# Kernel optimization log

Hardware: AMD Instinct MI355X
Metric: run time of the kernel (lower is better)

Reference implementation:

```python
import jax, jax.numpy as jnp
import numpy as np

IN_C, HID, LSTM_H, OUT_C = 128, 128, 128, 2
N_NODES, N_EDGES, N_GRAPHS = 100000, 1600000, 256


def gcn_conv(x, src, dst, W, b, n_nodes):
    # h = XW, then symmetric-normalized aggregation with self loops (PyG GCNConv defaults)
    h = x @ W  # [N, H]
    loop = jnp.arange(n_nodes)
    s = jnp.concatenate([src, loop])
    d = jnp.concatenate([dst, loop])
    deg = jax.ops.segment_sum(jnp.ones_like(d, dtype=h.dtype), d, num_segments=n_nodes)
    dinv = jnp.where(deg > 0, jax.lax.rsqrt(deg), 0.0)
    norm = dinv[s] * dinv[d]  # [E+N]
    out = jax.ops.segment_sum(norm[:, None] * h[s], d, num_segments=n_nodes)
    return out + b


def setup_inputs() -> dict:
    key = jax.random.key(0)
    ks = jax.random.split(key, 16)
    x = jax.random.normal(ks[0], (N_NODES, IN_C), dtype=jnp.float32)
    edge_index = jax.random.randint(ks[1], (2, N_EDGES), 0, N_NODES)
    batch = jnp.sort(jax.random.randint(ks[2], (N_NODES,), 0, N_GRAPHS))
    sc = lambda *shape: 1.0 / np.sqrt(shape[0])
    W0 = jax.random.normal(ks[3], (IN_C, HID), jnp.float32) * sc(IN_C)
    b0 = jnp.zeros((HID,), jnp.float32)
    W1 = jax.random.normal(ks[4], (HID, HID), jnp.float32) * sc(HID)
    b1 = jnp.zeros((HID,), jnp.float32)
    W2 = jax.random.normal(ks[5], (HID, HID), jnp.float32) * sc(HID)
    b2 = jnp.zeros((HID,), jnp.float32)
    W_ih = jax.random.normal(ks[6], (4 * LSTM_H, HID), jnp.float32) * sc(HID)
    W_hh = jax.random.normal(ks[7], (4 * LSTM_H, LSTM_H), jnp.float32) * sc(LSTM_H)
    b_ih = jnp.zeros((4 * LSTM_H,), jnp.float32)
    b_hh = jnp.zeros((4 * LSTM_H,), jnp.float32)
    W_fc = jax.random.normal(ks[8], (OUT_C, LSTM_H), jnp.float32) * sc(LSTM_H)
    b_fc = jnp.zeros((OUT_C,), jnp.float32)
    return dict(x=x, edge_index=edge_index, batch=batch, num_graphs=N_GRAPHS,
                W0=W0, b0=b0, W1=W1, b1=b1, W2=W2, b2=b2,
                W_ih=W_ih, W_hh=W_hh, b_ih=b_ih, b_hh=b_hh, W_fc=W_fc, b_fc=b_fc)


def reference(x, edge_index, batch, num_graphs, W0, b0, W1, b1, W2, b2,
              W_ih, W_hh, b_ih, b_hh, W_fc, b_fc):
    n_nodes = x.shape[0]
    src, dst = edge_index[0], edge_index[1]
    h = x
    for W, b in ((W0, b0), (W1, b1), (W2, b2)):
        h = jax.nn.relu(gcn_conv(h, src, dst, W, b, n_nodes))
    # dropout: identity in eval mode
    # global_mean_pool over batch ids
    sums = jax.ops.segment_sum(h, batch, num_segments=num_graphs)  # [G, HID]
    cnts = jax.ops.segment_sum(jnp.ones((n_nodes,), h.dtype), batch, num_segments=num_graphs)
    pooled = sums / jnp.maximum(cnts, 1.0)[:, None]
    # single-step LSTM from zero state: h0 = c0 = 0 => W_hh contributes 0
    g = pooled @ W_ih.T + b_ih + b_hh  # [G, 4H]
    i, f, gg, o = jnp.split(g, 4, axis=-1)  # PyTorch gate order i,f,g,o
    c = jax.nn.sigmoid(i) * jnp.tanh(gg)
    hn = jax.nn.sigmoid(o) * jnp.tanh(c)
    return hn @ W_fc.T + b_fc
```

## Files before the change

kernel.cpp:

```cpp
#include <hip/hip_runtime.h>
#include <math.h>
#include <stdint.h>

#define HID 128
#define SCAN_CHUNK 1024
#define NBUCK_MAX 512
#define EDGE_TILE 8192
#define GEMM_ROWS 128
#define XS_STRIDE 136

typedef short bf16x8 __attribute__((ext_vector_type(8)));
typedef float f32x4 __attribute__((ext_vector_type(4)));

__device__ __forceinline__ unsigned int f2bf(float f) {
    union { float f; uint32_t i; } u; u.f = f;
    uint32_t r = u.i + 0x7fffu + ((u.i >> 16) & 1u);
    return r >> 16;
}

__global__ __launch_bounds__(256) void scan_phase1(const int* __restrict__ cnt,
                                                   int* __restrict__ blockSums,
                                                   float* __restrict__ dinv, int nN) {
    __shared__ int sdata[256];
    const int t = threadIdx.x;
    const int idx = blockIdx.x * SCAN_CHUNK + t * 4;
    int v0 = 0, v1 = 0, v2 = 0, v3 = 0;
    if (idx + 3 < nN) {
        int4 v = *(const int4*)(cnt + idx);
        v0 = v.x; v1 = v.y; v2 = v.z; v3 = v.w;
        float4 dv;
        dv.x = rsqrtf((float)v0 + 1.0f);
        dv.y = rsqrtf((float)v1 + 1.0f);
        dv.z = rsqrtf((float)v2 + 1.0f);
        dv.w = rsqrtf((float)v3 + 1.0f);
        *(float4*)(dinv + idx) = dv;
    } else {
        if (idx     < nN) { v0 = cnt[idx];     dinv[idx]     = rsqrtf((float)v0 + 1.0f); }
        if (idx + 1 < nN) { v1 = cnt[idx + 1]; dinv[idx + 1] = rsqrtf((float)v1 + 1.0f); }
        if (idx + 2 < nN) { v2 = cnt[idx + 2]; dinv[idx + 2] = rsqrtf((float)v2 + 1.0f); }
        if (idx + 3 < nN) { v3 = cnt[idx + 3]; dinv[idx + 3] = rsqrtf((float)v3 + 1.0f); }
    }
    sdata[t] = v0 + v1 + v2 + v3;
    __syncthreads();
#pragma unroll
    for (int off = 128; off > 0; off >>= 1) {
        if (t < off) sdata[t] += sdata[t + off];
        __syncthreads();
    }
    if (t == 0) blockSums[blockIdx.x] = sdata[0];
}

__global__ __launch_bounds__(256) void scan_phase2(int* __restrict__ blockSums, int nB) {
    __shared__ int sd[256];
    const int t = threadIdx.x;
    sd[t] = (t < nB) ? blockSums[t] : 0;
    __syncthreads();
#pragma unroll
    for (int off = 1; off < 256; off <<= 1) {
        int v = sd[t];
        int add = (t >= off) ? sd[t - off] : 0;
        __syncthreads();
        sd[t] = v + add;
        __syncthreads();
    }
    if (t < nB) blockSums[t] = (t > 0) ? sd[t - 1] : 0;
}

__global__ __launch_bounds__(256) void scan_phase3(const int* __restrict__ cnt,
                                                   const int* __restrict__ blockOffsets,
                                                   int* __restrict__ rowptr, int nN, int nE) {
    __shared__ int sdata[256];
    const int t = threadIdx.x;
    const int idx = blockIdx.x * SCAN_CHUNK + t * 4;
    int v0 = 0, v1 = 0, v2 = 0, v3 = 0;
    if (idx + 3 < nN) {
        int4 v = *(const int4*)(cnt + idx);
        v0 = v.x; v1 = v.y; v2 = v.z; v3 = v.w;
    } else {
        if (idx     < nN) v0 = cnt[idx];
        if (idx + 1 < nN) v1 = cnt[idx + 1];
        if (idx + 2 < nN) v2 = cnt[idx + 2];
        if (idx + 3 < nN) v3 = cnt[idx + 3];
    }
    sdata[t] = v0 + v1 + v2 + v3;
    __syncthreads();
#pragma unroll
    for (int off = 1; off < 256; off <<= 1) {
        int v = sdata[t];
        int add = (t >= off) ? sdata[t - off] : 0;
        __syncthreads();
        sdata[t] = v + add;
        __syncthreads();
    }
    const int pre = blockOffsets[blockIdx.x] + ((t > 0) ? sdata[t - 1] : 0);
    if (idx + 3 < nN) {
        *(int4*)(rowptr + idx) = make_int4(pre, pre + v0, pre + v0 + v1, pre + v0 + v1 + v2);
    } else {
        if (idx     < nN) rowptr[idx]     = pre;
        if (idx + 1 < nN) rowptr[idx + 1] = pre + v0;
        if (idx + 2 < nN) rowptr[idx + 2] = pre + v0 + v1;
        if (idx + 3 < nN) rowptr[idx + 3] = pre + v0 + v1 + v2;
    }
    if (blockIdx.x == 0 && t == 0) rowptr[nN] = nE;
}

__global__ __launch_bounds__(256) void bucket_count(const int* __restrict__ dst,
                                                    int* __restrict__ bcnt, int nE, int nB) {
    __shared__ int h[NBUCK_MAX];
    for (int i = threadIdx.x; i < nB; i += 256) h[i] = 0;
    __syncthreads();
    const int base = blockIdx.x * EDGE_TILE;
    const int end = min(base + EDGE_TILE, nE);
    for (int e = base + threadIdx.x; e < end; e += 256)
        atomicAdd(&h[dst[e] >> 8], 1);
    __syncthreads();
    for (int i = threadIdx.x; i < nB; i += 256)
        if (h[i]) atomicAdd(&bcnt[i], h[i]);
}

__global__ __launch_bounds__(512) void bucket_scan(const int* __restrict__ bcnt,
                                                   int* __restrict__ boff,
                                                   int* __restrict__ bcur, int nB) {
    __shared__ int sd[512];
    const int t = threadIdx.x;
    sd[t] = (t < nB) ? bcnt[t] : 0;
    __syncthreads();
#pragma unroll
    for (int off = 1; off < 512; off <<= 1) {
        int v = sd[t];
        int add = (t >= off) ? sd[t - off] : 0;
        __syncthreads();
        sd[t] = v + add;
        __syncthreads();
    }
    if (t < nB) {
        int ex = (t > 0) ? sd[t - 1] : 0;
        boff[t] = ex;
        bcur[t] = ex;
    }
}

__global__ __launch_bounds__(256) void bucket_scatter(const int* __restrict__ src,
                                                      const int* __restrict__ dst,
                                                      int* __restrict__ bcur,
                                                      uint2* __restrict__ ebuf, int nE, int nB) {
    __shared__ int h[NBUCK_MAX];
    __shared__ int basearr[NBUCK_MAX];
    const int base = blockIdx.x * EDGE_TILE;
    const int end = min(base + EDGE_TILE, nE);
    for (int i = threadIdx.x; i < nB; i += 256) h[i] = 0;
    __syncthreads();
    for (int e = base + threadIdx.x; e < end; e += 256)
        atomicAdd(&h[dst[e] >> 8], 1);
    __syncthreads();
    for (int i = threadIdx.x; i < nB; i += 256) {
        int c = h[i];
        basearr[i] = c ? atomicAdd(&bcur[i], c) : 0;
        h[i] = 0;
    }
    __syncthreads();
    for (int e = base + threadIdx.x; e < end; e += 256) {
        int d = dst[e];
        int b = d >> 8;
        int pos = basearr[b] + atomicAdd(&h[b], 1);
        ebuf[pos] = make_uint2((unsigned)src[e], (unsigned)d);
    }
}

__global__ __launch_bounds__(256) void node_count(const uint2* __restrict__ ebuf,
                                                  const int* __restrict__ boff,
                                                  int* __restrict__ cnt, int nE, int nB, int nN) {
    __shared__ int h[256];
    h[threadIdx.x] = 0;
    __syncthreads();
    const int b = blockIdx.x;
    const int e0 = boff[b];
    const int e1 = (b + 1 < nB) ? boff[b + 1] : nE;
    for (int e = e0 + threadIdx.x; e < e1; e += 256)
        atomicAdd(&h[ebuf[e].y & 255], 1);
    __syncthreads();
    const int v = b * 256 + threadIdx.x;
    if (v < nN) cnt[v] = h[threadIdx.x];
}

__global__ __launch_bounds__(256) void csr_from_buckets(const uint2* __restrict__ ebuf,
                                                        const int* __restrict__ boff,
                                                        const int* __restrict__ rowptr,
                                                        int* __restrict__ ssrc, int nE, int nB) {
    __shared__ int cur[256];
    const int b = blockIdx.x;
    const int e0 = boff[b];
    const int e1 = (b + 1 < nB) ? boff[b + 1] : nE;
    cur[threadIdx.x] = 0;
    __syncthreads();
    for (int e = e0 + threadIdx.x; e < e1; e += 256) {
        uint2 ed = ebuf[e];
        int d = (int)ed.y;
        int pos = rowptr[d] + atomicAdd(&cur[d & 255], 1);
        ssrc[pos] = (int)ed.x;
    }
}

__global__ __launch_bounds__(256) void xcvt_kernel(const float* __restrict__ x,
                                                   uint4* __restrict__ Xb, int total) {
    int i = blockIdx.x * 256 + threadIdx.x;
    if (i < total) {
        const float4* xp = (const float4*)x + (size_t)i * 2;
        float4 u = xp[0], v = xp[1];
        uint4 o;
        o.x = f2bf(u.x) | (f2bf(u.y) << 16);
        o.y = f2bf(u.z) | (f2bf(u.w) << 16);
        o.z = f2bf(v.x) | (f2bf(v.y) << 16);
        o.w = f2bf(v.z) | (f2bf(v.w) << 16);
        Xb[i] = o;
    }
}

__global__ __launch_bounds__(256) void wt_kernel(const float* __restrict__ W0,
                                                 const float* __restrict__ W1,
                                                 const float* __restrict__ W2,
                                                 unsigned short* __restrict__ Wtb) {
    int i = blockIdx.x * 256 + threadIdx.x;
    if (i < 3 * HID * HID) {
        int w = i >> 14, r = i & 16383;
        int n = r >> 7, k = r & 127;
        const float* W = (w == 0) ? W0 : (w == 1) ? W1 : W2;
        Wtb[i] = (unsigned short)f2bf(W[k * HID + n]);
    }
}

__global__ __launch_bounds__(256) void gemm_mfma_kernel(const uint4* __restrict__ Xb,
                                                        const uint4* __restrict__ Wtb,
                                                        const float* __restrict__ dinv,
                                                        unsigned int* __restrict__ Pb32,
                                                        int nN) {
    __shared__ short Xs[GEMM_ROWS * XS_STRIDE];
    __shared__ short Ws[HID * XS_STRIDE];
    const int tid = threadIdx.x;
    const int rowBase = blockIdx.x * GEMM_ROWS;
#pragma unroll
    for (int it = 0; it < 8; ++it) {
        int f = it * 256 + tid;
        int row = f >> 4, c = f & 15;
        uint4 v = Xb[(size_t)(rowBase + row) * 16 + c];
        *(uint4*)(&Xs[row * XS_STRIDE + c * 8]) = v;
    }
#pragma unroll
    for (int it = 0; it < 8; ++it) {
        int f = it * 256 + tid;
        int n = f >> 4, c = f & 15;
        *(uint4*)(&Ws[n * XS_STRIDE + c * 8]) = Wtb[f];
    }
    __syncthreads();
    const int wave = tid >> 6, lane = tid & 63;
    const int quad = lane >> 4, l16 = lane & 15;
    f32x4 acc[2][8] = {};
    const int kq = quad * 8;
#pragma unroll
    for (int ks = 0; ks < 4; ++ks) {
        const int k0 = ks * 32 + kq;
        bf16x8 a0 = *(const bf16x8*)(&Xs[(wave * 32 + l16) * XS_STRIDE + k0]);
        bf16x8 a1 = *(const bf16x8*)(&Xs[(wave * 32 + 16 + l16) * XS_STRIDE + k0]);
#pragma unroll
        for (int nt = 0; nt < 8; ++nt) {
            bf16x8 b = *(const bf16x8*)(&Ws[(nt * 16 + l16) * XS_STRIDE + k0]);
            acc[0][nt] = __builtin_amdgcn_mfma_f32_16x16x32_bf16(a0, b, acc[0][nt], 0, 0, 0);
            acc[1][nt] = __builtin_amdgcn_mfma_f32_16x16x32_bf16(a1, b, acc[1][nt], 0, 0, 0);
        }
    }
#pragma unroll
    for (int mt = 0; mt < 2; ++mt) {
        const int gr0 = rowBase + wave * 32 + mt * 16 + quad * 4;
#pragma unroll
        for (int r = 0; r < 4; ++r) {
            const int gr = gr0 + r;
            const bool ok = gr < nN;
            const float d = ok ? dinv[gr] : 0.f;
#pragma unroll
            for (int nt = 0; nt < 8; ++nt) {
                float v = d * acc[mt][nt][r];
                float vo = __shfl_xor(v, 1, 64);
                if (ok && !(l16 & 1)) {
                    Pb32[(size_t)gr * 64 + nt * 8 + (l16 >> 1)] = f2bf(v) | (f2bf(vo) << 16);
                }
            }
        }
    }
}

__device__ __forceinline__ void acc_bf8(const uint4 q, float* a) {
    union { uint32_t i; float f; } t;
    t.i = q.x << 16;          a[0] += t.f;
    t.i = q.x & 0xffff0000u;  a[1] += t.f;
    t.i = q.y << 16;          a[2] += t.f;
    t.i = q.y & 0xffff0000u;  a[3] += t.f;
    t.i = q.z << 16;          a[4] += t.f;
    t.i = q.z & 0xffff0000u;  a[5] += t.f;
    t.i = q.w << 16;          a[6] += t.f;
    t.i = q.w & 0xffff0000u;  a[7] += t.f;
}

__global__ __launch_bounds__(256) void agg_kernel(const uint4* __restrict__ Pb,
                                                  const int* __restrict__ rowptr,
                                                  const int* __restrict__ ssrc,
                                                  const float* __restrict__ dinv,
                                                  const float* __restrict__ bias,
                                                  uint4* __restrict__ Xb_out, int nN) {
    const int lane = threadIdx.x & 15;
    const int grp = threadIdx.x >> 4;
    const int v = blockIdx.x * 16 + grp;
    if (v >= nN) return;
    float a0[8], a1[8], a2[8], a3[8];
#pragma unroll
    for (int i = 0; i < 8; ++i) { a0[i] = 0.f; a1[i] = 0.f; a2[i] = 0.f; a3[i] = 0.f; }
    acc_bf8(Pb[(size_t)v * 16 + lane], a0);
    int e = rowptr[v];
    const int e1 = rowptr[v + 1];
    for (; e + 4 <= e1; e += 4) {
        const int u0 = ssrc[e + 0], u1 = ssrc[e + 1], u2 = ssrc[e + 2], u3 = ssrc[e + 3];
        uint4 q0 = Pb[(size_t)u0 * 16 + lane];
        uint4 q1 = Pb[(size_t)u1 * 16 + lane];
        uint4 q2 = Pb[(size_t)u2 * 16 + lane];
        uint4 q3 = Pb[(size_t)u3 * 16 + lane];
        acc_bf8(q0, a0); acc_bf8(q1, a1); acc_bf8(q2, a2); acc_bf8(q3, a3);
    }
    for (; e < e1; ++e) {
        uint4 q = Pb[(size_t)ssrc[e] * 16 + lane];
        acc_bf8(q, a1);
    }
    const float dv = dinv[v];
    const float4 bb0 = ((const float4*)bias)[lane * 2];
    const float4 bb1 = ((const float4*)bias)[lane * 2 + 1];
    float4 o0, o1;
    o0.x = fmaxf(fmaf(dv, (a0[0] + a1[0]) + (a2[0] + a3[0]), bb0.x), 0.f);
    o0.y = fmaxf(fmaf(dv, (a0[1] + a1[1]) + (a2[1] + a3[1]), bb0.y), 0.f);
    o0.z = fmaxf(fmaf(dv, (a0[2] + a1[2]) + (a2[2] + a3[2]), bb0.z), 0.f);
    o0.w = fmaxf(fmaf(dv, (a0[3] + a1[3]) + (a2[3] + a3[3]), bb0.w), 0.f);
    o1.x = fmaxf(fmaf(dv, (a0[4] + a1[4]) + (a2[4] + a3[4]), bb1.x), 0.f);
    o1.y = fmaxf(fmaf(dv, (a0[5] + a1[5]) + (a2[5] + a3[5]), bb1.y), 0.f);
    o1.z = fmaxf(fmaf(dv, (a0[6] + a1[6]) + (a2[6] + a3[6]), bb1.z), 0.f);
    o1.w = fmaxf(fmaf(dv, (a0[7] + a1[7]) + (a2[7] + a3[7]), bb1.w), 0.f);
    uint4 q;
    q.x = f2bf(o0.x) | (f2bf(o0.y) << 16);
    q.y = f2bf(o0.z) | (f2bf(o0.w) << 16);
    q.z = f2bf(o1.x) | (f2bf(o1.y) << 16);
    q.w = f2bf(o1.z) | (f2bf(o1.w) << 16);
    Xb_out[(size_t)v * 16 + lane] = q;
}

__global__ __launch_bounds__(256) void pool_partial(const unsigned int* __restrict__ Xb32,
                                                    const int* __restrict__ batch,
                                                    float* __restrict__ psum, int nN) {
    const int c2 = threadIdx.x & 63;
    int n = blockIdx.x * 64 + (threadIdx.x >> 6);
    const int nEnd = min(blockIdx.x * 64 + 64, nN);
    float acc0 = 0.f, acc1 = 0.f;
    int g = -1;
    for (; n < nEnd; n += 4) {
        int gn = batch[n];
        unsigned int q = Xb32[(size_t)n * 64 + c2];
        union { uint32_t i; float f; } lo, hi;
        lo.i = q << 16; hi.i = q & 0xffff0000u;
        if (gn != g) {
            if (g >= 0) {
                atomicAdd(&psum[g * HID + c2 * 2], acc0);
                atomicAdd(&psum[g * HID + c2 * 2 + 1], acc1);
            }
            g = gn;
            acc0 = lo.f; acc1 = hi.f;
        } else {
            acc0 += lo.f; acc1 += hi.f;
        }
    }
    if (g >= 0) {
        atomicAdd(&psum[g * HID + c2 * 2], acc0);
        atomicAdd(&psum[g * HID + c2 * 2 + 1], acc1);
    }
}

__global__ __launch_bounds__(128) void pool_finalize(const float* __restrict__ psum,
                                                     const int* __restrict__ batch,
                                                     float* __restrict__ pooled, int nN) {
    const int g = blockIdx.x;
    int lo = 0, hi = nN;
    while (lo < hi) { int m = (lo + hi) >> 1; if (batch[m] < g) lo = m + 1; else hi = m; }
    const int start = lo;
    hi = nN;
    while (lo < hi) { int m = (lo + hi) >> 1; if (batch[m] < g + 1) lo = m + 1; else hi = m; }
    const float c = (float)max(lo - start, 1);
    pooled[g * HID + threadIdx.x] = psum[g * HID + threadIdx.x] / c;
}

__device__ __forceinline__ float sigmoidf_(float x) { return 1.0f / (1.0f + expf(-x)); }

__global__ __launch_bounds__(128) void lstm_fc_kernel(const float* __restrict__ pooled,
                                                      const float* __restrict__ W_ih,
                                                      const float* __restrict__ b_ih,
                                                      const float* __restrict__ b_hh,
                                                      const float* __restrict__ W_fc,
                                                      const float* __restrict__ b_fc,
                                                      float* __restrict__ out) {
    __shared__ float pv[HID];
    __shared__ float r0[2], r1[2];
    const int g = blockIdx.x, j = threadIdx.x;
    pv[j] = pooled[g * HID + j];
    __syncthreads();
    float di = b_ih[j] + b_hh[j];
    float dg = b_ih[256 + j] + b_hh[256 + j];
    float dO = b_ih[384 + j] + b_hh[384 + j];
    const float4* pv4 = (const float4*)pv;
#pragma unroll 4
    for (int k4 = 0; k4 < 32; ++k4) {
        float4 p = pv4[k4];
        float4 wi = *(const float4*)(W_ih + (size_t)j * HID + k4 * 4);
        float4 wg = *(const float4*)(W_ih + (size_t)(256 + j) * HID + k4 * 4);
        float4 wo = *(const float4*)(W_ih + (size_t)(384 + j) * HID + k4 * 4);
        di += p.x * wi.x + p.y * wi.y + p.z * wi.z + p.w * wi.w;
        dg += p.x * wg.x + p.y * wg.y + p.z * wg.z + p.w * wg.w;
        dO += p.x * wo.x + p.y * wo.y + p.z * wo.z + p.w * wo.w;
    }
    float c = sigmoidf_(di) * tanhf(dg);
    float hn = sigmoidf_(dO) * tanhf(c);
    float p0 = hn * W_fc[j];
    float p1 = hn * W_fc[HID + j];
#pragma unroll
    for (int off = 32; off > 0; off >>= 1) {
        p0 += __shfl_down(p0, off, 64);
        p1 += __shfl_down(p1, off, 64);
    }
    const int w = j >> 6, l = j & 63;
    if (l == 0) { r0[w] = p0; r1[w] = p1; }
    __syncthreads();
    if (j == 0) {
        out[g * 2 + 0] = r0[0] + r0[1] + b_fc[0];
        out[g * 2 + 1] = r1[0] + r1[1] + b_fc[1];
    }
}

extern "C" void kernel_launch(void* const* d_in, const int* in_sizes, int n_in,
                              void* d_out, int out_size, void* d_ws, size_t ws_size,
                              hipStream_t stream) {
    const float* x      = (const float*)d_in[0];
    const int*   eidx   = (const int*)d_in[1];
    const int*   batch  = (const int*)d_in[2];
    const float* W0     = (const float*)d_in[4];
    const float* b0     = (const float*)d_in[5];
    const float* W1     = (const float*)d_in[6];
    const float* b1     = (const float*)d_in[7];
    const float* W2     = (const float*)d_in[8];
    const float* b2     = (const float*)d_in[9];
    const float* W_ih   = (const float*)d_in[10];
    const float* b_ih   = (const float*)d_in[12];
    const float* b_hh   = (const float*)d_in[13];
    const float* W_fc   = (const float*)d_in[14];
    const float* b_fc   = (const float*)d_in[15];
    float* out = (float*)d_out;

    const int nN = in_sizes[0] / HID;
    const int nE = in_sizes[1] / 2;
    const int nG = out_size / 2;
    const int* src = eidx;
    const int* dst = eidx + nE;
    const int rowsPad = (nN + GEMM_ROWS - 1) & ~(GEMM_ROWS - 1);

    size_t off = 0;
    auto alloc = [&](size_t bytes) -> void* {
        void* p = (char*)d_ws + off;
        off += (bytes + 255) & ~(size_t)255;
        return p;
    };
    uint4* Pb     = (uint4*)alloc((size_t)rowsPad * 16 * sizeof(uint4));
    uint4* Xb     = (uint4*)alloc((size_t)nN * 16 * sizeof(uint4));
    float* dinv   = (float*)alloc((size_t)nN * sizeof(float));
    int*   cnt    = (int*)alloc((size_t)nN * sizeof(int));
    int*   rowptr = (int*)alloc((size_t)(nN + 1) * sizeof(int));
    int*   ssrc   = (int*)alloc((size_t)nE * sizeof(int));
    uint2* ebuf   = (uint2*)alloc((size_t)nE * sizeof(uint2));
    float* pooled = (float*)alloc((size_t)nG * HID * sizeof(float));
    float* psum   = (float*)alloc((size_t)nG * HID * sizeof(float));
    int*   blockSums = (int*)alloc(1024 * sizeof(int));
    int*   bcnt   = (int*)alloc(NBUCK_MAX * sizeof(int));
    int*   boff   = (int*)alloc(NBUCK_MAX * sizeof(int));
    int*   bcur   = (int*)alloc(NBUCK_MAX * sizeof(int));
    unsigned short* Wtb = (unsigned short*)alloc(3 * HID * HID * sizeof(unsigned short));
    (void)ws_size;

    const int scanBlocks = (nN + SCAN_CHUNK - 1) / SCAN_CHUNK;
    const int nB = (nN + 255) >> 8;
    const int tileBlocks = (nE + EDGE_TILE - 1) / EDGE_TILE;

    hipMemsetAsync(bcnt, 0, NBUCK_MAX * sizeof(int), stream);
    bucket_count<<<tileBlocks, 256, 0, stream>>>(dst, bcnt, nE, nB);
    bucket_scan<<<1, 512, 0, stream>>>(bcnt, boff, bcur, nB);
    bucket_scatter<<<tileBlocks, 256, 0, stream>>>(src, dst, bcur, ebuf, nE, nB);

    node_count<<<nB, 256, 0, stream>>>(ebuf, boff, cnt, nE, nB, nN);
    scan_phase1<<<scanBlocks, 256, 0, stream>>>(cnt, blockSums, dinv, nN);
    scan_phase2<<<1, 256, 0, stream>>>(blockSums, scanBlocks);
    scan_phase3<<<scanBlocks, 256, 0, stream>>>(cnt, blockSums, rowptr, nN, nE);
    csr_from_buckets<<<nB, 256, 0, stream>>>(ebuf, boff, rowptr, ssrc, nE, nB);

    const int xTotal = nN * 16;
    xcvt_kernel<<<(xTotal + 255) / 256, 256, 0, stream>>>(x, Xb, xTotal);
    wt_kernel<<<(3 * HID * HID + 255) / 256, 256, 0, stream>>>(W0, W1, W2, Wtb);

    const int gemmBlocks = rowsPad / GEMM_ROWS;
    const int aggBlocks = (nN + 15) / 16;
    const uint4* Wt0 = (const uint4*)Wtb;
    const uint4* Wt1 = (const uint4*)(Wtb + HID * HID);
    const uint4* Wt2 = (const uint4*)(Wtb + 2 * HID * HID);

    gemm_mfma_kernel<<<gemmBlocks, 256, 0, stream>>>(Xb, Wt0, dinv, (unsigned int*)Pb, nN);
    agg_kernel<<<aggBlocks, 256, 0, stream>>>(Pb, rowptr, ssrc, dinv, b0, Xb, nN);
    gemm_mfma_kernel<<<gemmBlocks, 256, 0, stream>>>(Xb, Wt1, dinv, (unsigned int*)Pb, nN);
    agg_kernel<<<aggBlocks, 256, 0, stream>>>(Pb, rowptr, ssrc, dinv, b1, Xb, nN);
    gemm_mfma_kernel<<<gemmBlocks, 256, 0, stream>>>(Xb, Wt2, dinv, (unsigned int*)Pb, nN);
    agg_kernel<<<aggBlocks, 256, 0, stream>>>(Pb, rowptr, ssrc, dinv, b2, Xb, nN);

    hipMemsetAsync(psum, 0, (size_t)nG * HID * sizeof(float), stream);
    pool_partial<<<(nN + 63) / 64, 256, 0, stream>>>((const unsigned int*)Xb, batch, psum, nN);
    pool_finalize<<<nG, 128, 0, stream>>>(psum, batch, pooled, nN);
    lstm_fc_kernel<<<nG, 128, 0, stream>>>(pooled, W_ih, b_ih, b_hh, W_fc, b_fc, out);
}
```

Measured before the change: 480.3 us.

## Split CSR neighbors by source half and fuse fp32-to-bf16 conversion into first GEMM

The CSR build now sorts each node's neighbor list into two segments, sources in the lower half of node ids and sources in the upper half, and records a per-node midpoint. The aggregation kernel walks the lower-half segment first and then the upper half, so gathers across all concurrently running waves concentrate on one half of the feature table at a time, aiming for better L2/MALL locality. The separate x-to-bf16 conversion kernel is removed, and a new first-layer GEMM reads the fp32 input and converts it while loading into shared memory; the GEMM also gains bounds checks on rows. The cost is an extra counting pass over edges in the CSR build, an extra rowmid array, and an outer loop in aggregation that may leave more remainder iterations.

```diff
diff --git a/kernel.cpp b/kernel.cpp
--- a/kernel.cpp
+++ b/kernel.cpp
@@ -186,33 +186,38 @@
 __global__ __launch_bounds__(256) void csr_from_buckets(const uint2* __restrict__ ebuf,
                                                         const int* __restrict__ boff,
                                                         const int* __restrict__ rowptr,
-                                                        int* __restrict__ ssrc, int nE, int nB) {
-    __shared__ int cur[256];
+                                                        int* __restrict__ rowmid,
+                                                        int* __restrict__ ssrc,
+                                                        int nE, int nB, int nN, int nHalf) {
+    __shared__ int rbase[256];
+    __shared__ int rmid[256];
+    __shared__ int cLow[256], cHigh[256];
+    const int t = threadIdx.x;
     const int b = blockIdx.x;
     const int e0 = boff[b];
     const int e1 = (b + 1 < nB) ? boff[b + 1] : nE;
-    cur[threadIdx.x] = 0;
-    __syncthreads();
-    for (int e = e0 + threadIdx.x; e < e1; e += 256) {
+    const int v = b * 256 + t;
+    rbase[t] = (v <= nN) ? rowptr[v] : 0;
+    cLow[t] = 0;
+    __syncthreads();
+    for (int e = e0 + t; e < e1; e += 256) {
         uint2 ed = ebuf[e];
-        int d = (int)ed.y;
-        int pos = rowptr[d] + atomicAdd(&cur[d & 255], 1);
-        ssrc[pos] = (int)ed.x;
-    }
-}
-
-__global__ __launch_bounds__(256) void xcvt_kernel(const float* __restrict__ x,
-                                                   uint4* __restrict__ Xb, int total) {
-    int i = blockIdx.x * 256 + threadIdx.x;
-    if (i < total) {
-        const float4* xp = (const float4*)x + (size_t)i * 2;
-        float4 u = xp[0], v = xp[1];
-        uint4 o;
-        o.x = f2bf(u.x) | (f2bf(u.y) << 16);
-        o.y = f2bf(u.z) | (f2bf(u.w) << 16);
-        o.z = f2bf(v.x) | (f2bf(v.y) << 16);
-        o.w = f2bf(v.z) | (f2bf(v.w) << 16);
-        Xb[i] = o;
+        if ((int)ed.x < nHalf) atomicAdd(&cLow[ed.y & 255], 1);
+    }
+    __syncthreads();
+    rmid[t] = rbase[t] + cLow[t];
+    if (v < nN) rowmid[v] = rmid[t];
+    cLow[t] = 0;
+    cHigh[t] = 0;
+    __syncthreads();
+    for (int e = e0 + t; e < e1; e += 256) {
+        uint2 ed = ebuf[e];
+        int li = (int)ed.y & 255;
+        int u = (int)ed.x;
+        int pos;
+        if (u < nHalf) pos = rbase[li] + atomicAdd(&cLow[li], 1);
+        else           pos = rmid[li] + atomicAdd(&cHigh[li], 1);
+        ssrc[pos] = u;
     }
 }
 
@@ -242,8 +247,74 @@
     for (int it = 0; it < 8; ++it) {
         int f = it * 256 + tid;
         int row = f >> 4, c = f & 15;
-        uint4 v = Xb[(size_t)(rowBase + row) * 16 + c];
+        int grow = rowBase + row;
+        uint4 v = make_uint4(0u, 0u, 0u, 0u);
+        if (grow < nN) v = Xb[(size_t)grow * 16 + c];
         *(uint4*)(&Xs[row * XS_STRIDE + c * 8]) = v;
+    }
+#pragma unroll
+    for (int it = 0; it < 8; ++it) {
+        int f = it * 256 + tid;
+        int n = f >> 4, c = f & 15;
+        *(uint4*)(&Ws[n * XS_STRIDE + c * 8]) = Wtb[f];
+    }
+    __syncthreads();
+    const int wave = tid >> 6, lane = tid & 63;
+    const int quad = lane >> 4, l16 = lane & 15;
+    f32x4 acc[2][8] = {};
+    const int kq = quad * 8;
+#pragma unroll
+    for (int ks = 0; ks < 4; ++ks) {
+        const int k0 = ks * 32 + kq;
+        bf16x8 a0 = *(const bf16x8*)(&Xs[(wave * 32 + l16) * XS_STRIDE + k0]);
+        bf16x8 a1 = *(const bf16x8*)(&Xs[(wave * 32 + 16 + l16) * XS_STRIDE + k0]);
+#pragma unroll
+        for (int nt = 0; nt < 8; ++nt) {
+            bf16x8 b = *(const bf16x8*)(&Ws[(nt * 16 + l16) * XS_STRIDE + k0]);
+            acc[0][nt] = __builtin_amdgcn_mfma_f32_16x16x32_bf16(a0, b, acc[0][nt], 0, 0, 0);
+            acc[1][nt] = __builtin_amdgcn_mfma_f32_16x16x32_bf16(a1, b, acc[1][nt], 0, 0, 0);
+        }
+    }
+#pragma unroll
+    for (int mt = 0; mt < 2; ++mt) {
+        const int gr0 = rowBase + wave * 32 + mt * 16 + quad * 4;
+#pragma unroll
+        for (int r = 0; r < 4; ++r) {
+            const int gr = gr0 + r;
+            const bool ok = gr < nN;
+            const float d = ok ? dinv[gr] : 0.f;
+#pragma unroll
+            for (int nt = 0; nt < 8; ++nt) {
+                float v = d * acc[mt][nt][r];
+                float vo = __shfl_xor(v, 1, 64);
+                if (ok && !(l16 & 1)) {
+                    Pb32[(size_t)gr * 64 + nt * 8 + (l16 >> 1)] = f2bf(v) | (f2bf(vo) << 16);
+                }
+            }
+        }
+    }
+}
+
+__global__ __launch_bounds__(256) void gemm_mfma_f32in(const float* __restrict__ X,
+                                                       const uint4* __restrict__ Wtb,
+                                                       const float* __restrict__ dinv,
+                                                       unsigned int* __restrict__ Pb32,
+                                                       int nN) {
+    __shared__ short Xs[GEMM_ROWS * XS_STRIDE];
+    __shared__ short Ws[HID * XS_STRIDE];
+    const int tid = threadIdx.x;
+    const int rowBase = blockIdx.x * GEMM_ROWS;
+#pragma unroll
+    for (int it = 0; it < 16; ++it) {
+        int f = it * 256 + tid;
+        int row = f >> 5, c = f & 31;
+        int grow = rowBase + row;
+        float4 v = make_float4(0.f, 0.f, 0.f, 0.f);
+        if (grow < nN) v = *(const float4*)(X + (size_t)grow * HID + c * 4);
+        uint2 o;
+        o.x = f2bf(v.x) | (f2bf(v.y) << 16);
+        o.y = f2bf(v.z) | (f2bf(v.w) << 16);
+        *(uint2*)(&Xs[row * XS_STRIDE + c * 4]) = o;
     }
 #pragma unroll
     for (int it = 0; it < 8; ++it) {
@@ -302,6 +373,7 @@
 
 __global__ __launch_bounds__(256) void agg_kernel(const uint4* __restrict__ Pb,
                                                   const int* __restrict__ rowptr,
+                                                  const int* __restrict__ rowmid,
                                                   const int* __restrict__ ssrc,
                                                   const float* __restrict__ dinv,
                                                   const float* __restrict__ bias,
@@ -314,19 +386,23 @@
 #pragma unroll
     for (int i = 0; i < 8; ++i) { a0[i] = 0.f; a1[i] = 0.f; a2[i] = 0.f; a3[i] = 0.f; }
     acc_bf8(Pb[(size_t)v * 16 + lane], a0);
-    int e = rowptr[v];
-    const int e1 = rowptr[v + 1];
-    for (; e + 4 <= e1; e += 4) {
-        const int u0 = ssrc[e + 0], u1 = ssrc[e + 1], u2 = ssrc[e + 2], u3 = ssrc[e + 3];
-        uint4 q0 = Pb[(size_t)u0 * 16 + lane];
-        uint4 q1 = Pb[(size_t)u1 * 16 + lane];
-        uint4 q2 = Pb[(size_t)u2 * 16 + lane];
-        uint4 q3 = Pb[(size_t)u3 * 16 + lane];
-        acc_bf8(q0, a0); acc_bf8(q1, a1); acc_bf8(q2, a2); acc_bf8(q3, a3);
-    }
-    for (; e < e1; ++e) {
-        uint4 q = Pb[(size_t)ssrc[e] * 16 + lane];
-        acc_bf8(q, a1);
+    const int ee0 = rowptr[v], em = rowmid[v], ee1 = rowptr[v + 1];
+#pragma unroll 1
+    for (int ph = 0; ph < 2; ++ph) {
+        int e = ph ? em : ee0;
+        const int eE = ph ? ee1 : em;
+        for (; e + 4 <= eE; e += 4) {
+            const int u0 = ssrc[e + 0], u1 = ssrc[e + 1], u2 = ssrc[e + 2], u3 = ssrc[e + 3];
+            uint4 q0 = Pb[(size_t)u0 * 16 + lane];
+            uint4 q1 = Pb[(size_t)u1 * 16 + lane];
+            uint4 q2 = Pb[(size_t)u2 * 16 + lane];
+            uint4 q3 = Pb[(size_t)u3 * 16 + lane];
+            acc_bf8(q0, a0); acc_bf8(q1, a1); acc_bf8(q2, a2); acc_bf8(q3, a3);
+        }
+        for (; e < eE; ++e) {
+            uint4 q = Pb[(size_t)ssrc[e] * 16 + lane];
+            acc_bf8(q, a1);
+        }
     }
     const float dv = dinv[v];
     const float4 bb0 = ((const float4*)bias)[lane * 2];
@@ -462,6 +538,7 @@
     const int* src = eidx;
     const int* dst = eidx + nE;
     const int rowsPad = (nN + GEMM_ROWS - 1) & ~(GEMM_ROWS - 1);
+    const int nHalf = nN >> 1;
 
     size_t off = 0;
     auto alloc = [&](size_t bytes) -> void* {
@@ -474,6 +551,7 @@
     float* dinv   = (float*)alloc((size_t)nN * sizeof(float));
     int*   cnt    = (int*)alloc((size_t)nN * sizeof(int));
     int*   rowptr = (int*)alloc((size_t)(nN + 1) * sizeof(int));
+    int*   rowmid = (int*)alloc((size_t)nN * sizeof(int));
     int*   ssrc   = (int*)alloc((size_t)nE * sizeof(int));
     uint2* ebuf   = (uint2*)alloc((size_t)nE * sizeof(uint2));
     float* pooled = (float*)alloc((size_t)nG * HID * sizeof(float));
@@ -498,10 +576,8 @@
     scan_phase1<<<scanBlocks, 256, 0, stream>>>(cnt, blockSums, dinv, nN);
     scan_phase2<<<1, 256, 0, stream>>>(blockSums, scanBlocks);
     scan_phase3<<<scanBlocks, 256, 0, stream>>>(cnt, blockSums, rowptr, nN, nE);
-    csr_from_buckets<<<nB, 256, 0, stream>>>(ebuf, boff, rowptr, ssrc, nE, nB);
-
-    const int xTotal = nN * 16;
-    xcvt_kernel<<<(xTotal + 255) / 256, 256, 0, stream>>>(x, Xb, xTotal);
+    csr_from_buckets<<<nB, 256, 0, stream>>>(ebuf, boff, rowptr, rowmid, ssrc, nE, nB, nN, nHalf);
+
     wt_kernel<<<(3 * HID * HID + 255) / 256, 256, 0, stream>>>(W0, W1, W2, Wtb);
 
     const int gemmBlocks = rowsPad / GEMM_ROWS;
@@ -510,12 +586,12 @@
     const uint4* Wt1 = (const uint4*)(Wtb + HID * HID);
     const uint4* Wt2 = (const uint4*)(Wtb + 2 * HID * HID);
 
-    gemm_mfma_kernel<<<gemmBlocks, 256, 0, stream>>>(Xb, Wt0, dinv, (unsigned int*)Pb, nN);
-    agg_kernel<<<aggBlocks, 256, 0, stream>>>(Pb, rowptr, ssrc, dinv, b0, Xb, nN);
+    gemm_mfma_f32in<<<gemmBlocks, 256, 0, stream>>>(x, Wt0, dinv, (unsigned int*)Pb, nN);
+    agg_kernel<<<aggBlocks, 256, 0, stream>>>(Pb, rowptr, rowmid, ssrc, dinv, b0, Xb, nN);
     gemm_mfma_kernel<<<gemmBlocks, 256, 0, stream>>>(Xb, Wt1, dinv, (unsigned int*)Pb, nN);
-    agg_kernel<<<aggBlocks, 256, 0, stream>>>(Pb, rowptr, ssrc, dinv, b1, Xb, nN);
+    agg_kernel<<<aggBlocks, 256, 0, stream>>>(Pb, rowptr, rowmid, ssrc, dinv, b1, Xb, nN);
     gemm_mfma_kernel<<<gemmBlocks, 256, 0, stream>>>(Xb, Wt2, dinv, (unsigned int*)Pb, nN);
-    agg_kernel<<<aggBlocks, 256, 0, stream>>>(Pb, rowptr, ssrc, dinv, b2, Xb, nN);
+    agg_kernel<<<aggBlocks, 256, 0, stream>>>(Pb, rowptr, rowmid, ssrc, dinv, b2, Xb, nN);
 
     hipMemsetAsync(psum, 0, (size_t)nG * HID * sizeof(float), stream);
     pool_partial<<<(nN + 63) / 64, 256, 0, stream>>>((const unsigned int*)Xb, batch, psum, nN);
```

Measured after the change: 478.6 us. No clear change (-0.4%).

## Fuse aggregation with next-layer GEMM, fold x conversion into GEMM, pack edge buffer

Applied to the files above, without the earlier changes.

The first GEMM now reads fp32 x and converts it to bf16 while staging, so the separate x conversion pass is gone. Layers 1 and 2 fuse the neighbour aggregation, bias and ReLU with the next layer's MFMA GEMM through a 16-row shared tile, which avoids writing and re-reading the intermediate activations. Ping-pong buffers Pb and Pb2 hold the projected features. Edge bucketing packs src<<8 | local dst into one 32-bit word, halving ebuf traffic, but this assumes source ids fit in 24 bits. Each fused block reloads the full 128x128 weight tile and runs only a small MFMA, adding per-block overhead.

```diff
diff --git a/kernel.cpp b/kernel.cpp
--- a/kernel.cpp
+++ b/kernel.cpp
@@ -143,7 +143,8 @@
 __global__ __launch_bounds__(256) void bucket_scatter(const int* __restrict__ src,
                                                       const int* __restrict__ dst,
                                                       int* __restrict__ bcur,
-                                                      uint2* __restrict__ ebuf, int nE, int nB) {
+                                                      unsigned int* __restrict__ ebuf,
+                                                      int nE, int nB) {
     __shared__ int h[NBUCK_MAX];
     __shared__ int basearr[NBUCK_MAX];
     const int base = blockIdx.x * EDGE_TILE;
@@ -163,11 +164,11 @@
         int d = dst[e];
         int b = d >> 8;
         int pos = basearr[b] + atomicAdd(&h[b], 1);
-        ebuf[pos] = make_uint2((unsigned)src[e], (unsigned)d);
-    }
-}
-
-__global__ __launch_bounds__(256) void node_count(const uint2* __restrict__ ebuf,
+        ebuf[pos] = ((unsigned)src[e] << 8) | ((unsigned)d & 255u);
+    }
+}
+
+__global__ __launch_bounds__(256) void node_count(const unsigned int* __restrict__ ebuf,
                                                   const int* __restrict__ boff,
                                                   int* __restrict__ cnt, int nE, int nB, int nN) {
     __shared__ int h[256];
@@ -177,13 +178,13 @@
     const int e0 = boff[b];
     const int e1 = (b + 1 < nB) ? boff[b + 1] : nE;
     for (int e = e0 + threadIdx.x; e < e1; e += 256)
-        atomicAdd(&h[ebuf[e].y & 255], 1);
+        atomicAdd(&h[ebuf[e] & 255u], 1);
     __syncthreads();
     const int v = b * 256 + threadIdx.x;
     if (v < nN) cnt[v] = h[threadIdx.x];
 }
 
-__global__ __launch_bounds__(256) void csr_from_buckets(const uint2* __restrict__ ebuf,
+__global__ __launch_bounds__(256) void csr_from_buckets(const unsigned int* __restrict__ ebuf,
                                                         const int* __restrict__ boff,
                                                         const int* __restrict__ rowptr,
                                                         int* __restrict__ ssrc, int nE, int nB) {
@@ -191,28 +192,14 @@
     const int b = blockIdx.x;
     const int e0 = boff[b];
     const int e1 = (b + 1 < nB) ? boff[b + 1] : nE;
+    const int nodeBase = b * 256;
     cur[threadIdx.x] = 0;
     __syncthreads();
     for (int e = e0 + threadIdx.x; e < e1; e += 256) {
-        uint2 ed = ebuf[e];
-        int d = (int)ed.y;
-        int pos = rowptr[d] + atomicAdd(&cur[d & 255], 1);
-        ssrc[pos] = (int)ed.x;
-    }
-}
-
-__global__ __launch_bounds__(256) void xcvt_kernel(const float* __restrict__ x,
-                                                   uint4* __restrict__ Xb, int total) {
-    int i = blockIdx.x * 256 + threadIdx.x;
-    if (i < total) {
-        const float4* xp = (const float4*)x + (size_t)i * 2;
-        float4 u = xp[0], v = xp[1];
-        uint4 o;
-        o.x = f2bf(u.x) | (f2bf(u.y) << 16);
-        o.y = f2bf(u.z) | (f2bf(u.w) << 16);
-        o.z = f2bf(v.x) | (f2bf(v.y) << 16);
-        o.w = f2bf(v.z) | (f2bf(v.w) << 16);
-        Xb[i] = o;
+        unsigned int ed = ebuf[e];
+        int li = (int)(ed & 255u);
+        int pos = rowptr[nodeBase + li] + atomicAdd(&cur[li], 1);
+        ssrc[pos] = (int)(ed >> 8);
     }
 }
 
@@ -229,21 +216,26 @@
     }
 }
 
-__global__ __launch_bounds__(256) void gemm_mfma_kernel(const uint4* __restrict__ Xb,
-                                                        const uint4* __restrict__ Wtb,
-                                                        const float* __restrict__ dinv,
-                                                        unsigned int* __restrict__ Pb32,
-                                                        int nN) {
+__global__ __launch_bounds__(256) void gemm_mfma_f32in(const float* __restrict__ X,
+                                                       const uint4* __restrict__ Wtb,
+                                                       const float* __restrict__ dinv,
+                                                       unsigned int* __restrict__ Pb32,
+                                                       int nN) {
     __shared__ short Xs[GEMM_ROWS * XS_STRIDE];
     __shared__ short Ws[HID * XS_STRIDE];
     const int tid = threadIdx.x;
     const int rowBase = blockIdx.x * GEMM_ROWS;
 #pragma unroll
-    for (int it = 0; it < 8; ++it) {
+    for (int it = 0; it < 16; ++it) {
         int f = it * 256 + tid;
-        int row = f >> 4, c = f & 15;
-        uint4 v = Xb[(size_t)(rowBase + row) * 16 + c];
-        *(uint4*)(&Xs[row * XS_STRIDE + c * 8]) = v;
+        int row = f >> 5, c = f & 31;
+        int grow = rowBase + row;
+        float4 v = make_float4(0.f, 0.f, 0.f, 0.f);
+        if (grow < nN) v = *(const float4*)(X + (size_t)grow * HID + c * 4);
+        uint2 o;
+        o.x = f2bf(v.x) | (f2bf(v.y) << 16);
+        o.y = f2bf(v.z) | (f2bf(v.w) << 16);
+        *(uint2*)(&Xs[row * XS_STRIDE + c * 4]) = o;
     }
 #pragma unroll
     for (int it = 0; it < 8; ++it) {
@@ -298,6 +290,96 @@
     t.i = q.z & 0xffff0000u;  a[5] += t.f;
     t.i = q.w << 16;          a[6] += t.f;
     t.i = q.w & 0xffff0000u;  a[7] += t.f;
+}
+
+__global__ __launch_bounds__(256) void fused_agg_gemm(const uint4* __restrict__ Pb,
+                                                      const int* __restrict__ rowptr,
+                                                      const int* __restrict__ ssrc,
+                                                      const float* __restrict__ dinv,
+                                                      const float* __restrict__ bias,
+                                                      const uint4* __restrict__ Wtb,
+                                                      unsigned int* __restrict__ Pout32,
+                                                      int nN) {
+    __shared__ short Ws[HID * XS_STRIDE];
+    __shared__ short Hs[16 * XS_STRIDE];
+    const int tid = threadIdx.x;
+#pragma unroll
+    for (int it = 0; it < 8; ++it) {
+        int f = it * 256 + tid;
+        int n = f >> 4, c = f & 15;
+        *(uint4*)(&Ws[n * XS_STRIDE + c * 8]) = Wtb[f];
+    }
+    const int lane16 = tid & 15;
+    const int grp = tid >> 4;
+    const int v = blockIdx.x * 16 + grp;
+    const bool ok = v < nN;
+    float a0[8], a1[8], a2[8], a3[8];
+#pragma unroll
+    for (int i = 0; i < 8; ++i) { a0[i] = 0.f; a1[i] = 0.f; a2[i] = 0.f; a3[i] = 0.f; }
+    uint4 q = make_uint4(0u, 0u, 0u, 0u);
+    if (ok) {
+        acc_bf8(Pb[(size_t)v * 16 + lane16], a0);
+        int e = rowptr[v];
+        const int e1 = rowptr[v + 1];
+        for (; e + 4 <= e1; e += 4) {
+            const int u0 = ssrc[e + 0], u1 = ssrc[e + 1], u2 = ssrc[e + 2], u3 = ssrc[e + 3];
+            uint4 q0 = Pb[(size_t)u0 * 16 + lane16];
+            uint4 q1 = Pb[(size_t)u1 * 16 + lane16];
+            uint4 q2 = Pb[(size_t)u2 * 16 + lane16];
+            uint4 q3 = Pb[(size_t)u3 * 16 + lane16];
+            acc_bf8(q0, a0); acc_bf8(q1, a1); acc_bf8(q2, a2); acc_bf8(q3, a3);
+        }
+        for (; e < e1; ++e) {
+            uint4 qe = Pb[(size_t)ssrc[e] * 16 + lane16];
+            acc_bf8(qe, a1);
+        }
+        const float dv = dinv[v];
+        const float4 bb0 = ((const float4*)bias)[lane16 * 2];
+        const float4 bb1 = ((const float4*)bias)[lane16 * 2 + 1];
+        float4 o0, o1;
+        o0.x = fmaxf(fmaf(dv, (a0[0] + a1[0]) + (a2[0] + a3[0]), bb0.x), 0.f);
+        o0.y = fmaxf(fmaf(dv, (a0[1] + a1[1]) + (a2[1] + a3[1]), bb0.y), 0.f);
+        o0.z = fmaxf(fmaf(dv, (a0[2] + a1[2]) + (a2[2] + a3[2]), bb0.z), 0.f);
+        o0.w = fmaxf(fmaf(dv, (a0[3] + a1[3]) + (a2[3] + a3[3]), bb0.w), 0.f);
+        o1.x = fmaxf(fmaf(dv, (a0[4] + a1[4]) + (a2[4] + a3[4]), bb1.x), 0.f);
+        o1.y = fmaxf(fmaf(dv, (a0[5] + a1[5]) + (a2[5] + a3[5]), bb1.y), 0.f);
+        o1.z = fmaxf(fmaf(dv, (a0[6] + a1[6]) + (a2[6] + a3[6]), bb1.z), 0.f);
+        o1.w = fmaxf(fmaf(dv, (a0[7] + a1[7]) + (a2[7] + a3[7]), bb1.w), 0.f);
+        q.x = f2bf(o0.x) | (f2bf(o0.y) << 16);
+        q.y = f2bf(o0.z) | (f2bf(o0.w) << 16);
+        q.z = f2bf(o1.x) | (f2bf(o1.y) << 16);
+        q.w = f2bf(o1.z) | (f2bf(o1.w) << 16);
+    }
+    *(uint4*)(&Hs[grp * XS_STRIDE + lane16 * 8]) = q;
+    __syncthreads();
+    const int wave = tid >> 6, lane = tid & 63;
+    const int quad = lane >> 4, l16 = lane & 15;
+    f32x4 acc[2] = {};
+#pragma unroll
+    for (int ks = 0; ks < 4; ++ks) {
+        const int k0 = ks * 32 + quad * 8;
+        bf16x8 a = *(const bf16x8*)(&Hs[l16 * XS_STRIDE + k0]);
+#pragma unroll
+        for (int nt = 0; nt < 2; ++nt) {
+            bf16x8 b = *(const bf16x8*)(&Ws[((wave * 2 + nt) * 16 + l16) * XS_STRIDE + k0]);
+            acc[nt] = __builtin_amdgcn_mfma_f32_16x16x32_bf16(a, b, acc[nt], 0, 0, 0);
+        }
+    }
+#pragma unroll
+    for (int r = 0; r < 4; ++r) {
+        const int gr = blockIdx.x * 16 + quad * 4 + r;
+        const bool okr = gr < nN;
+        const float d = okr ? dinv[gr] : 0.f;
+#pragma unroll
+        for (int nt = 0; nt < 2; ++nt) {
+            float val = d * acc[nt][r];
+            float vo = __shfl_xor(val, 1, 64);
+            if (okr && !(l16 & 1)) {
+                Pout32[(size_t)gr * 64 + (wave * 2 + nt) * 8 + (l16 >> 1)] =
+                    f2bf(val) | (f2bf(vo) << 16);
+            }
+        }
+    }
 }
 
 __global__ __launch_bounds__(256) void agg_kernel(const uint4* __restrict__ Pb,
@@ -469,13 +551,14 @@
         off += (bytes + 255) & ~(size_t)255;
         return p;
     };
-    uint4* Pb     = (uint4*)alloc((size_t)rowsPad * 16 * sizeof(uint4));
+    uint4* Pb     = (uint4*)alloc((size_t)nN * 16 * sizeof(uint4));
+    uint4* Pb2    = (uint4*)alloc((size_t)nN * 16 * sizeof(uint4));
     uint4* Xb     = (uint4*)alloc((size_t)nN * 16 * sizeof(uint4));
     float* dinv   = (float*)alloc((size_t)nN * sizeof(float));
     int*   cnt    = (int*)alloc((size_t)nN * sizeof(int));
     int*   rowptr = (int*)alloc((size_t)(nN + 1) * sizeof(int));
     int*   ssrc   = (int*)alloc((size_t)nE * sizeof(int));
-    uint2* ebuf   = (uint2*)alloc((size_t)nE * sizeof(uint2));
+    unsigned int* ebuf = (unsigned int*)alloc((size_t)nE * sizeof(unsigned int));
     float* pooled = (float*)alloc((size_t)nG * HID * sizeof(float));
     float* psum   = (float*)alloc((size_t)nG * HID * sizeof(float));
     int*   blockSums = (int*)alloc(1024 * sizeof(int));
@@ -500,21 +583,19 @@
     scan_phase3<<<scanBlocks, 256, 0, stream>>>(cnt, blockSums, rowptr, nN, nE);
     csr_from_buckets<<<nB, 256, 0, stream>>>(ebuf, boff, rowptr, ssrc, nE, nB);
 
-    const int xTotal = nN * 16;
-    xcvt_kernel<<<(xTotal + 255) / 256, 256, 0, stream>>>(x, Xb, xTotal);
     wt_kernel<<<(3 * HID * HID + 255) / 256, 256, 0, stream>>>(W0, W1, W2, Wtb);
 
     const int gemmBlocks = rowsPad / GEMM_ROWS;
     const int aggBlocks = (nN + 15) / 16;
-    const uint4* Wt0 = (const uint4*)Wtb;
     const uint4* Wt1 = (const uint4*)(Wtb + HID * HID);
     const uint4* Wt2 = (const uint4*)(Wtb + 2 * HID * HID);
 
-    gemm_mfma_kernel<<<gemmBlocks, 256, 0, stream>>>(Xb, Wt0, dinv, (unsigned int*)Pb, nN);
-    agg_kernel<<<aggBlocks, 256, 0, stream>>>(Pb, rowptr, ssrc, dinv, b0, Xb, nN);
-    gemm_mfma_kernel<<<gemmBlocks, 256, 0, stream>>>(Xb, Wt1, dinv, (unsigned int*)Pb, nN);
-    agg_kernel<<<aggBlocks, 256, 0, stream>>>(Pb, rowptr, ssrc, dinv, b1, Xb, nN);
-    gemm_mfma_kernel<<<gemmBlocks, 256, 0, stream>>>(Xb, Wt2, dinv, (unsigned int*)Pb, nN);
+    gemm_mfma_f32in<<<gemmBlocks, 256, 0, stream>>>(x, (const uint4*)Wtb, dinv,
+                                                    (unsigned int*)Pb, nN);
+    fused_agg_gemm<<<aggBlocks, 256, 0, stream>>>(Pb, rowptr, ssrc, dinv, b0, Wt1,
+                                                  (unsigned int*)Pb2, nN);
+    fused_agg_gemm<<<aggBlocks, 256, 0, stream>>>(Pb2, rowptr, ssrc, dinv, b1, Wt2,
+                                                  (unsigned int*)Pb, nN);
     agg_kernel<<<aggBlocks, 256, 0, stream>>>(Pb, rowptr, ssrc, dinv, b2, Xb, nN);
 
     hipMemsetAsync(psum, 0, (size_t)nG * HID * sizeof(float), stream);
```

Result: faster. 466.2 us (-2.9%).
